# Kernel optimization log

Measured on AMD Instinct MI355X. Metric: run time of the kernel, lower is better.

The kernel has to match this reference:

```python
import jax, jax.numpy as jnp
import numpy as np

CH = 1024
NH = 16
HD = CH // NH


def setup_inputs() -> dict:
    key = jax.random.key(0)
    k1, k2, k3 = jax.random.split(key, 3)
    x = jax.random.normal(k1, (8, 1024, CH), dtype=jnp.float32)
    # torch.nn.Linear weights are [out, in]; store as [in, out] for x @ W
    s = 1.0 / np.sqrt(CH)
    W_qkv = jax.random.uniform(k2, (CH, 3 * CH), dtype=jnp.float32, minval=-s, maxval=s)
    W_out = jax.random.uniform(k3, (CH, CH), dtype=jnp.float32, minval=-s, maxval=s)
    return {"x": x, "W_qkv": W_qkv, "W_out": W_out}


def reference(x, W_qkv, W_out):
    B, N, C = x.shape
    qkv = x @ W_qkv                                   # [B, N, 3C]
    q, k, v = jnp.split(qkv, 3, axis=-1)
    # [B, N, C] -> [B, H, N, D]
    def heads(t):
        return t.reshape(B, N, NH, HD).transpose(0, 2, 1, 3)
    q, k, v = heads(q), heads(k), heads(v)
    scale = 1.0 / np.sqrt(HD).astype(np.float32)
    scores = jnp.einsum('bhqd,bhkd->bhqk', q, k) * scale
    attn = jax.nn.softmax(scores, axis=-1)
    out = jnp.einsum('bhqk,bhkd->bhqd', attn, v)      # [B, H, N, D]
    out = out.transpose(0, 2, 1, 3).reshape(B, N, C)
    return out @ W_out
```

## Files before the change

kernel.cpp:

```cpp
#include <hip/hip_runtime.h>
#include <math.h>

#define NH 16
#define HD 64

typedef unsigned short u16;
typedef unsigned int   u32;
using bf16x8 = __attribute__((ext_vector_type(8))) short;
using f32x4  = __attribute__((ext_vector_type(4))) float;
using u16x8  = __attribute__((ext_vector_type(8))) unsigned short;
using u16x4  = __attribute__((ext_vector_type(4))) unsigned short;
using u32x2  = __attribute__((ext_vector_type(2))) unsigned int;

__device__ __forceinline__ u16 f2bf(float x) {
    u32 u = __float_as_uint(x);
    u32 r = (u + 0x7FFFu + ((u >> 16) & 1u)) >> 16;
    return (u16)r;
}
__device__ __forceinline__ float bf2f(u16 h) { return __uint_as_float(((u32)h) << 16); }

#define GLDS16(src, dst) __builtin_amdgcn_global_load_lds( \
    (const __attribute__((address_space(1))) void*)(src),  \
    (__attribute__((address_space(3))) void*)(dst), 16, 0, 0)

#define LDS_OFF(p) ((u32)(uintptr_t)(__attribute__((address_space(3))) void*)(p))
#define DSREAD(d, a) asm volatile("ds_read_b128 %0, %1" : "=v"(d) : "v"(a))

#define MEMFENCE asm volatile("" ::: "memory")
#define BARMID { MEMFENCE; __builtin_amdgcn_s_barrier(); \
                 asm volatile("s_waitcnt lgkmcnt(0)" ::: "memory"); \
                 __builtin_amdgcn_sched_barrier(0); }
#define BAREND { MEMFENCE; __builtin_amdgcn_s_barrier(); MEMFENCE; }
#define VMW(n) asm volatile("s_waitcnt vmcnt(" #n ")" ::: "memory")

__global__ __launch_bounds__(256) void convert_x(const float* __restrict__ x,
                                                 u16* __restrict__ xt) {
    int t = blockIdx.x * 256 + threadIdx.x;
    int m = t >> 7;
    int k = (t & 127) * 8;
    const float4* src = (const float4*)(x + (size_t)m * 1024 + k);
    float4 v0 = src[0], v1 = src[1];
    float vs[8] = {v0.x, v0.y, v0.z, v0.w, v1.x, v1.y, v1.z, v1.w};
    u16x8 hv;
    #pragma unroll
    for (int j = 0; j < 8; j++) hv[j] = f2bf(vs[j]);
    *(u16x8*)(xt + (size_t)m * 1024 + k) = hv;
}

__global__ __launch_bounds__(256) void conv_w(const float* __restrict__ W,
                                              u16* __restrict__ wqk,
                                              u16* __restrict__ wv) {
    __shared__ float Ts[32][33];
    const int N = 3072;
    int k0 = blockIdx.y * 32, n0 = blockIdx.x * 32;
    int t = threadIdx.x;
    int r = t >> 3, c4 = (t & 7) * 4;
    float4 v = *(const float4*)(W + (size_t)(k0 + r) * N + n0 + c4);
    Ts[r][c4] = v.x; Ts[r][c4 + 1] = v.y; Ts[r][c4 + 2] = v.z; Ts[r][c4 + 3] = v.w;
    __syncthreads();
    int nl = t >> 3, kl = (t & 7) * 4;
    u16x4 hv;
    #pragma unroll
    for (int j = 0; j < 4; j++) hv[j] = f2bf(Ts[kl + j][nl]);
    int col = n0 + nl;
    if (col < 2048) {
        *(u16x4*)&wqk[(size_t)col * 1024 + k0 + kl] = hv;
    } else {
        *(u16x4*)&wv[(size_t)(col - 2048) * 1024 + k0 + kl] = hv;
    }
}

__global__ __launch_bounds__(256) void conv_wout(const float* __restrict__ W,
                                                 u16* __restrict__ Wt) {
    __shared__ float Ts[32][33];
    const int N = 1024;
    int k0 = blockIdx.y * 32, n0 = blockIdx.x * 32;
    int t = threadIdx.x;
    int r = t >> 3, c4 = (t & 7) * 4;
    float4 v = *(const float4*)(W + (size_t)(k0 + r) * N + n0 + c4);
    Ts[r][c4] = v.x; Ts[r][c4 + 1] = v.y; Ts[r][c4 + 2] = v.z; Ts[r][c4 + 3] = v.w;
    __syncthreads();
    int nl = t >> 3, kl = (t & 7) * 4;
    u16x4 hv;
    #pragma unroll
    for (int j = 0; j < 4; j++) hv[j] = f2bf(Ts[kl + j][nl]);
    *(u16x4*)&Wt[(size_t)(n0 + nl) * 1024 + k0 + kl] = hv;
}

__global__ __launch_bounds__(512, 2)
void gemm_qk_8ph(const u16* __restrict__ A, const u16* __restrict__ Bt,
                 u16* __restrict__ Qh, u16* __restrict__ Kh,
                 int Kp, int nbx) {
    __shared__ char LDS[131072];
    char* ldsA = LDS;
    char* ldsB = LDS + 65536;
    const u32 ldsAoff = LDS_OFF(ldsA);
    const u32 ldsBoff = ldsAoff + 65536;

    const int tid = threadIdx.x, lane = tid & 63, w = tid >> 6;
    const int wr = w >> 2, wc = w & 3;
    const int l15 = lane & 15;
    const int khb = (lane >> 4) << 4;
    const int lswz = (l15 & 7) << 4;
    const int Kp2 = Kp * 2;

    const int cpx = (int)gridDim.x >> 3;
    const int wg  = ((int)blockIdx.x & 7) * cpx + ((int)blockIdx.x >> 3);
    const int m0 = (wg / nbx) * 256, n0 = (wg % nbx) * 256;

    const int tp = tid >> 3;
    const int sw = ((tid & 7) * 16) ^ ((tp & 7) << 4);
    const int nA = ((tp >> 5) << 6) + (tp & 31);

    const char* Agb = (const char*)A  + (size_t)m0 * Kp2;
    const char* Bgb = (const char*)Bt + (size_t)n0 * Kp2;

#define STAGE_A(t, h, buf) { \
    const char* s_ = Agb + (t) * 128 + ((h) * 64 + tp) * Kp2 + sw; \
    char* d_ = ldsA + (buf) * 32768 + (h) * 16384 + (w << 10); \
    GLDS16(s_, d_); GLDS16(s_ + (size_t)128 * Kp2, d_ + 8192); }
#define STAGE_B(t, h, buf) { \
    const char* s_ = Bgb + (t) * 128 + (nA + (h) * 32) * Kp2 + sw; \
    char* d_ = ldsB + (buf) * 32768 + (h) * 16384 + (w << 10); \
    GLDS16(s_, d_); GLDS16(s_ + (size_t)128 * Kp2, d_ + 8192); }

    bf16x8 Af[4][2], Bf[2][2];

#define LOADA(buf, mh) { \
    _Pragma("unroll") \
    for (int mi = 0; mi < 4; ++mi) { \
        u32 rb_ = ldsAoff + (buf) * 32768 + (mh) * 16384 \
                + (u32)((wr * 64 + mi * 16 + l15) * 128); \
        DSREAD(Af[mi][0], rb_ + (u32)((khb) ^ lswz)); \
        DSREAD(Af[mi][1], rb_ + (u32)((64 + khb) ^ lswz)); \
    } }
#define LOADB(buf, nh) { \
    _Pragma("unroll") \
    for (int ni = 0; ni < 2; ++ni) { \
        u32 rb_ = ldsBoff + (buf) * 32768 + (nh) * 16384 \
                + (u32)((wc * 32 + ni * 16 + l15) * 128); \
        DSREAD(Bf[ni][0], rb_ + (u32)((khb) ^ lswz)); \
        DSREAD(Bf[ni][1], rb_ + (u32)((64 + khb) ^ lswz)); \
    } }
#define MM(mh, nh) { \
    __builtin_amdgcn_s_setprio(1); \
    _Pragma("unroll") \
    for (int kk = 0; kk < 2; ++kk) \
        _Pragma("unroll") \
        for (int mi = 0; mi < 4; ++mi) \
            _Pragma("unroll") \
            for (int ni = 0; ni < 2; ++ni) \
                acc[(mh) * 4 + mi][(nh) * 2 + ni] = \
                    __builtin_amdgcn_mfma_f32_16x16x32_bf16( \
                        Af[mi][kk], Bf[ni][kk], acc[(mh) * 4 + mi][(nh) * 2 + ni], 0, 0, 0); \
    __builtin_amdgcn_s_setprio(0); }

    f32x4 acc[8][4];
    #pragma unroll
    for (int i = 0; i < 8; i++)
        #pragma unroll
        for (int j = 0; j < 4; j++)
            acc[i][j] = f32x4{0.f, 0.f, 0.f, 0.f};

    const int NT = Kp >> 6;
    const int NITER = NT / 2 - 1;

    STAGE_B(0, 0, 0); STAGE_A(0, 1, 0); STAGE_B(0, 1, 0); STAGE_A(0, 0, 0);
    STAGE_B(1, 0, 1); STAGE_A(1, 1, 1); STAGE_B(1, 1, 1);
    VMW(6);
    MEMFENCE; __builtin_amdgcn_s_barrier(); MEMFENCE;

    for (int it = 0; it < NITER; ++it) {
        const int t = 2 * it;
        LOADA(0, 0); LOADB(0, 0); STAGE_A(t + 1, 0, 1);
        BARMID; MM(0, 0); BAREND;
        LOADA(0, 1); STAGE_B(t + 2, 0, 0);
        BARMID; MM(1, 0); BAREND;
        LOADB(0, 1); STAGE_A(t + 2, 1, 0);
        BARMID; MM(1, 1); BAREND;
        LOADA(0, 0); STAGE_B(t + 2, 1, 0); VMW(6);
        BARMID; MM(0, 1); BAREND;
        LOADA(1, 0); LOADB(1, 0); STAGE_A(t + 2, 0, 0);
        BARMID; MM(0, 0); BAREND;
        LOADA(1, 1); STAGE_B(t + 3, 0, 1);
        BARMID; MM(1, 0); BAREND;
        LOADB(1, 1); STAGE_A(t + 3, 1, 1);
        BARMID; MM(1, 1); BAREND;
        LOADA(1, 0); STAGE_B(t + 3, 1, 1); VMW(6);
        BARMID; MM(0, 1); BAREND;
    }

    LOADA(0, 0); LOADB(0, 0); STAGE_A(NT - 1, 0, 1);
    BARMID; MM(0, 0); BAREND;
    LOADA(0, 1);
    BARMID; MM(1, 0); BAREND;
    LOADB(0, 1);
    BARMID; MM(1, 1); BAREND;
    LOADA(0, 0); VMW(0);
    BARMID; MM(0, 1); BAREND;
    LOADA(1, 0); LOADB(1, 0);
    BARMID; MM(0, 0); BAREND;
    LOADA(1, 1);
    BARMID; MM(1, 0); BAREND;
    LOADB(1, 1);
    BARMID; MM(1, 1); BAREND;
    LOADA(1, 0);
    BARMID; MM(0, 1); BAREND;

    const int sel = n0 >> 10;
    u16* dst = (sel == 0) ? Qh : Kh;
    const float sc = (sel == 0) ? 0.125f : 1.0f;
    #pragma unroll
    for (int mh = 0; mh < 2; ++mh)
        #pragma unroll
        for (int mi = 0; mi < 4; ++mi)
            #pragma unroll
            for (int nh = 0; nh < 2; ++nh)
                #pragma unroll
                for (int ni = 0; ni < 2; ++ni) {
                    f32x4 a = acc[mh * 4 + mi][nh * 2 + ni];
                    int col = n0 + wc * 64 + nh * 32 + ni * 16 + l15;
                    int within = col & 1023;
                    int hh = within >> 6, d = within & 63;
                    int rowb = m0 + wr * 128 + mh * 64 + mi * 16 + (lane >> 4) * 4;
                    int bb = rowb >> 10, n = rowb & 1023;
                    size_t hn = (size_t)(bb * NH + hh) * 1024 + n;
                    #pragma unroll
                    for (int reg = 0; reg < 4; reg++)
                        dst[(hn + reg) * 64 + d] = f2bf(a[reg] * sc);
                }
#undef STAGE_A
#undef STAGE_B
#undef LOADA
#undef LOADB
#undef MM
}

template<int MODE>
__global__ __launch_bounds__(256, 2)
void gemm_bf16(const u16* __restrict__ A, int lda,
               const u16* __restrict__ Bt, int ldb, int Kloop,
               float* __restrict__ C, u16* __restrict__ Vtr, int N, int nbx) {
    __shared__ u16 As[128 * 64];
    __shared__ u16 Bs[128 * 64];
    const char* AsC = (const char*)As;
    const char* BsC = (const char*)Bs;

    const int t = threadIdx.x;
    const int lane = t & 63, w = t >> 6;

    const int cpx = (int)gridDim.x >> 3;
    const int wg  = (blockIdx.x & 7) * cpx + (blockIdx.x >> 3);
    const int m0 = (wg / nbx) * 128, n0 = (wg % nbx) * 128;

    const int l15 = lane & 15;
    const int g16 = (lane >> 4) << 4;
    const int swz = (l15 & 7) << 4;

    const char* srcA[4];
    const char* srcB[4];
    char* dstA[4];
    char* dstB[4];
    #pragma unroll
    for (int i = 0; i < 4; i++) {
        int s = (w * 4 + i) * 64 + lane;
        int row  = (s * 16) >> 7;
        int colb = (s * 16) & 127;
        int scol = colb ^ ((row & 7) << 4);
        srcA[i] = (const char*)A  + ((size_t)(m0 + row) * lda) * 2 + scol;
        srcB[i] = (const char*)Bt + ((size_t)(n0 + row) * ldb) * 2 + scol;
        dstA[i] = (char*)As + (w * 4 + i) * 1024;
        dstB[i] = (char*)Bs + (w * 4 + i) * 1024;
    }

    const int wm = (w >> 1) * 64, wn = (w & 1) * 64;
    int rA[4], rB[4];
    #pragma unroll
    for (int i = 0; i < 4; i++) {
        rA[i] = (wm + i * 16 + l15) * 128;
        rB[i] = (wn + i * 16 + l15) * 128;
    }

    f32x4 acc[4][4];
    #pragma unroll
    for (int i = 0; i < 4; i++)
        #pragma unroll
        for (int j = 0; j < 4; j++)
            acc[i][j] = f32x4{0.f, 0.f, 0.f, 0.f};

    for (int k0 = 0; k0 < Kloop; k0 += 64) {
        __syncthreads();
        #pragma unroll
        for (int i = 0; i < 4; i++) {
            GLDS16(srcA[i], dstA[i]);
            GLDS16(srcB[i], dstB[i]);
            srcA[i] += 128;
            srcB[i] += 128;
        }
        __syncthreads();
        #pragma unroll
        for (int kb = 0; kb < 2; kb++) {
            const int csw = ((kb << 6) | g16) ^ swz;
            bf16x8 af[4], bfr[4];
            #pragma unroll
            for (int mi = 0; mi < 4; mi++) af[mi]  = *(const bf16x8*)(AsC + rA[mi] + csw);
            #pragma unroll
            for (int ni = 0; ni < 4; ni++) bfr[ni] = *(const bf16x8*)(BsC + rB[ni] + csw);
            #pragma unroll
            for (int mi = 0; mi < 4; mi++)
                #pragma unroll
                for (int ni = 0; ni < 4; ni++)
                    acc[mi][ni] = __builtin_amdgcn_mfma_f32_16x16x32_bf16(
                        af[mi], bfr[ni], acc[mi][ni], 0, 0, 0);
        }
    }

    if (MODE == 0) {
        #pragma unroll
        for (int mi = 0; mi < 4; mi++) {
            int rowb = m0 + wm + mi * 16 + (lane >> 4) * 4;
            #pragma unroll
            for (int ni = 0; ni < 4; ni++) {
                int col = n0 + wn + ni * 16 + l15;
                #pragma unroll
                for (int reg = 0; reg < 4; reg++)
                    C[(size_t)(rowb + reg) * N + col] = acc[mi][ni][reg];
            }
        }
    } else {
        #pragma unroll
        for (int ni = 0; ni < 4; ni++) {
            int col = n0 + wn + ni * 16 + l15;
            int hh = col >> 6, d = col & 63;
            #pragma unroll
            for (int mi = 0; mi < 4; mi++) {
                int rowb = m0 + wm + mi * 16 + (lane >> 4) * 4;
                int bb = rowb >> 10, n = rowb & 1023;
                u16x4 vv;
                #pragma unroll
                for (int reg = 0; reg < 4; reg++)
                    vv[reg] = f2bf(acc[mi][ni][reg]);
                *(u16x4*)&Vtr[((size_t)(bb * NH + hh) * 64 + d) * 1024 + n] = vv;
            }
        }
    }
}

__global__ __launch_bounds__(256, 4)
void attn_mfma(const u16* __restrict__ Qh, const u16* __restrict__ Kh,
               const u16* __restrict__ Vt, u16* __restrict__ AO) {
    __shared__ u16 Ks[64 * 64];
    __shared__ u16 Vs[64 * 64];
    __shared__ u16 Ps[4][16 * 72];

    const int t = threadIdx.x, lane = t & 63, w = t >> 6;

    const int orig = blockIdx.x;
    const int xcd = orig & 7, slot = orig >> 3;
    const int head_lin = xcd * 16 + (slot >> 4);
    const int qt = slot & 15;
    const int b = head_lin >> 4, h = head_lin & 15;
    const size_t head = (size_t)head_lin;

    const char* Qg = (const char*)(Qh + head * 1024 * 64) + qt * 64 * 128;
    const char* Kg = (const char*)(Kh + head * 1024 * 64);
    const char* Vg = (const char*)(Vt + head * 64 * 1024);
    char* KsC = (char*)Ks;
    char* VsC = (char*)Vs;
    char* PsC = (char*)(&Ps[w][0]);

    const int l15 = lane & 15;
    const int g16 = (lane >> 4) << 4;
    const int g8  = (lane >> 4) << 3;
    const int swz = (l15 & 7) << 4;

    #pragma unroll
    for (int i = 0; i < 2; i++) {
        int c = (w * 2 + i) * 64 + lane;
        int row = c >> 3, colb = (c & 7) * 16;
        int off = row * 128 + (colb ^ ((row & 7) << 4));
        GLDS16(Kg + off, KsC + (w * 2 + i) * 1024);
        GLDS16(Vg + row * 2048 + (colb ^ ((row & 7) << 4)), VsC + (w * 2 + i) * 1024);
    }

    const int qrow = w * 16 + l15;
    bf16x8 qf[2];
    #pragma unroll
    for (int kk = 0; kk < 2; kk++)
        qf[kk] = *(const bf16x8*)(Qg + qrow * 128 + kk * 64 + g16);

    int ksrcoff[2], kdst[2], vsrcoff[2], vdst[2];
    #pragma unroll
    for (int i = 0; i < 2; i++) {
        int c = i * 256 + t;
        int row = c >> 3, colb = (c & 7) * 16;
        ksrcoff[i] = c * 16;
        kdst[i]    = row * 128 + (colb ^ ((row & 7) << 4));
        vsrcoff[i] = row * 2048 + colb;
        vdst[i]    = row * 128 + (colb ^ ((row & 7) << 4));
    }

    float lp = 0.f;
    f32x4 acc_o[4];
    #pragma unroll
    for (int i = 0; i < 4; i++) acc_o[i] = f32x4{0.f, 0.f, 0.f, 0.f};

    __syncthreads();

    for (int kt = 0; kt < 16; kt++) {
        u16x8 kst[2], vst[2];
        if (kt < 15) {
            const char* ks = Kg + (kt + 1) * 8192;
            const char* vs = Vg + (kt + 1) * 128;
            #pragma unroll
            for (int i = 0; i < 2; i++) {
                kst[i] = *(const u16x8*)(ks + ksrcoff[i]);
                vst[i] = *(const u16x8*)(vs + vsrcoff[i]);
            }
        }

        f32x4 sacc[4];
        #pragma unroll
        for (int c = 0; c < 4; c++) sacc[c] = f32x4{0.f, 0.f, 0.f, 0.f};
        __builtin_amdgcn_s_setprio(1);
        #pragma unroll
        for (int kk = 0; kk < 2; kk++) {
            int csw = ((kk * 64) | g16) ^ swz;
            #pragma unroll
            for (int c = 0; c < 4; c++) {
                bf16x8 bk = *(const bf16x8*)(KsC + (c * 16 + l15) * 128 + csw);
                sacc[c] = __builtin_amdgcn_mfma_f32_16x16x32_bf16(bk, qf[kk], sacc[c], 0, 0, 0);
            }
        }
        __builtin_amdgcn_s_setprio(0);

        {
            char* pb = PsC + l15 * 144 + g8;
            #pragma unroll
            for (int c = 0; c < 4; c++) {
                float p0 = __expf(sacc[c][0]);
                float p1 = __expf(sacc[c][1]);
                float p2 = __expf(sacc[c][2]);
                float p3 = __expf(sacc[c][3]);
                lp += (p0 + p1) + (p2 + p3);
                u32 w0, w1;
                asm("v_cvt_pk_bf16_f32 %0, %1, %2" : "=v"(w0) : "v"(p0), "v"(p1));
                asm("v_cvt_pk_bf16_f32 %0, %1, %2" : "=v"(w1) : "v"(p2), "v"(p3));
                u16x4 pk = __builtin_bit_cast(u16x4, u32x2{w0, w1});
                *(u16x4*)(pb + c * 32) = pk;
            }
        }
        MEMFENCE;
        asm volatile("s_waitcnt lgkmcnt(0)" ::: "memory");
        __builtin_amdgcn_sched_barrier(0);

        __builtin_amdgcn_s_setprio(1);
        #pragma unroll
        for (int kb = 0; kb < 2; kb++) {
            bf16x8 ap = *(const bf16x8*)(PsC + l15 * 144 + kb * 64 + g16);
            #pragma unroll
            for (int c2 = 0; c2 < 4; c2++) {
                int vrow = c2 * 16 + l15;
                int voff = vrow * 128 + (((kb << 6) | g16) ^ ((vrow & 7) << 4));
                bf16x8 bv = *(const bf16x8*)(VsC + voff);
                acc_o[c2] = __builtin_amdgcn_mfma_f32_16x16x32_bf16(ap, bv, acc_o[c2], 0, 0, 0);
            }
        }
        __builtin_amdgcn_s_setprio(0);

        __syncthreads();
        if (kt < 15) {
            #pragma unroll
            for (int i = 0; i < 2; i++) {
                *(u16x8*)(KsC + kdst[i]) = kst[i];
                *(u16x8*)(VsC + vdst[i]) = vst[i];
            }
            __syncthreads();
        }
    }

    lp += __shfl_xor(lp, 16, 64);
    lp += __shfl_xor(lp, 32, 64);
    float linv[4];
    #pragma unroll
    for (int reg = 0; reg < 4; reg++)
        linv[reg] = 1.0f / __shfl(lp, ((lane >> 4) << 2) + reg, 64);

    #pragma unroll
    for (int c2 = 0; c2 < 4; c2++) {
        int col = h * 64 + c2 * 16 + l15;
        #pragma unroll
        for (int reg = 0; reg < 4; reg++) {
            int row = b * 1024 + qt * 64 + w * 16 + (lane >> 4) * 4 + reg;
            float v = acc_o[c2][reg] * linv[reg];
            AO[(size_t)row * 1024 + col] = f2bf(v);
        }
    }
}

extern "C" void kernel_launch(void* const* d_in, const int* in_sizes, int n_in,
                              void* d_out, int out_size, void* d_ws, size_t ws_size,
                              hipStream_t stream) {
    const float* x    = (const float*)d_in[0];
    const float* Wqkv = (const float*)d_in[1];
    const float* Wout = (const float*)d_in[2];
    float* out = (float*)d_out;

    u16* xt    = (u16*)d_ws;
    u16* wqk   = xt + 8192ull * 1024;
    u16* wv    = wqk + 2048ull * 1024;
    u16* woutt = wv + 1024ull * 1024;
    u16* Qh    = woutt + 1024ull * 1024;
    u16* Kh    = Qh + 128ull * 1024 * 64;
    u16* Vtr   = Kh + 128ull * 1024 * 64;
    u16* AO    = xt;

    convert_x<<<4096, 256, 0, stream>>>(x, xt);
    conv_w<<<dim3(96, 32), 256, 0, stream>>>(Wqkv, wqk, wv);
    conv_wout<<<dim3(32, 32), 256, 0, stream>>>(Wout, woutt);

    gemm_qk_8ph<<<256, 512, 0, stream>>>(xt, wqk, Qh, Kh, 1024, 8);

    gemm_bf16<2><<<512, 256, 0, stream>>>(
        xt, 1024, wv, 1024, 1024, nullptr, Vtr, 1024, 8);

    attn_mfma<<<2048, 256, 0, stream>>>(Qh, Kh, Vtr, AO);

    gemm_bf16<0><<<512, 256, 0, stream>>>(
        AO, 1024, woutt, 1024, 1024, out, nullptr, 1024, 8);
}
```

Before: 154.4 us.

## Double-buffer attention K/V tiles with direct global-to-LDS loads and exp2 softmax

The attention kernel now keeps two LDS buffers for K and V. The next tile is fetched straight into the spare buffer with global_load_lds, replacing the old register staging plus an extra write-and-sync phase. This removes one barrier per iteration and the register round-trip, at the cost of twice the K/V shared memory, and the occupancy hint drops from 4 to 3 blocks. Separately, log2(e) is folded into the Q scaling in the projection kernel so the softmax can use exp2f instead of __expf.

```diff
diff --git a/kernel.cpp b/kernel.cpp
--- a/kernel.cpp
+++ b/kernel.cpp
@@ -209,7 +209,7 @@
 
     const int sel = n0 >> 10;
     u16* dst = (sel == 0) ? Qh : Kh;
-    const float sc = (sel == 0) ? 0.125f : 1.0f;
+    const float sc = (sel == 0) ? 0.125f * 1.4426950408889634f : 1.0f;
     #pragma unroll
     for (int mh = 0; mh < 2; ++mh)
         #pragma unroll
@@ -346,11 +346,11 @@
     }
 }
 
-__global__ __launch_bounds__(256, 4)
+__global__ __launch_bounds__(256, 3)
 void attn_mfma(const u16* __restrict__ Qh, const u16* __restrict__ Kh,
                const u16* __restrict__ Vt, u16* __restrict__ AO) {
-    __shared__ u16 Ks[64 * 64];
-    __shared__ u16 Vs[64 * 64];
+    __shared__ u16 Ks[2][64 * 64];
+    __shared__ u16 Vs[2][64 * 64];
     __shared__ u16 Ps[4][16 * 72];
 
     const int t = threadIdx.x, lane = t & 63, w = t >> 6;
@@ -372,16 +372,24 @@
     const int l15 = lane & 15;
     const int g16 = (lane >> 4) << 4;
     const int g8  = (lane >> 4) << 3;
-    const int swz = (l15 & 7) << 4;
-
+
+    int koff[2], vgoff[2], ldst[2];
     #pragma unroll
     for (int i = 0; i < 2; i++) {
         int c = (w * 2 + i) * 64 + lane;
         int row = c >> 3, colb = (c & 7) * 16;
-        int off = row * 128 + (colb ^ ((row & 7) << 4));
-        GLDS16(Kg + off, KsC + (w * 2 + i) * 1024);
-        GLDS16(Vg + row * 2048 + (colb ^ ((row & 7) << 4)), VsC + (w * 2 + i) * 1024);
-    }
+        int soff = colb ^ ((row & 7) << 4);
+        koff[i]  = row * 128 + soff;
+        vgoff[i] = row * 2048 + soff;
+        ldst[i]  = (w * 2 + i) * 1024;
+    }
+
+#define STAGE_KV(kt, buf) { \
+    _Pragma("unroll") \
+    for (int i = 0; i < 2; i++) { \
+        GLDS16(Kg + (kt) * 8192 + koff[i], KsC + (buf) * 8192 + ldst[i]); \
+        GLDS16(Vg + (kt) * 128  + vgoff[i], VsC + (buf) * 8192 + ldst[i]); \
+    } }
 
     const int qrow = w * 16 + l15;
     bf16x8 qf[2];
@@ -389,35 +397,17 @@
     for (int kk = 0; kk < 2; kk++)
         qf[kk] = *(const bf16x8*)(Qg + qrow * 128 + kk * 64 + g16);
 
-    int ksrcoff[2], kdst[2], vsrcoff[2], vdst[2];
-    #pragma unroll
-    for (int i = 0; i < 2; i++) {
-        int c = i * 256 + t;
-        int row = c >> 3, colb = (c & 7) * 16;
-        ksrcoff[i] = c * 16;
-        kdst[i]    = row * 128 + (colb ^ ((row & 7) << 4));
-        vsrcoff[i] = row * 2048 + colb;
-        vdst[i]    = row * 128 + (colb ^ ((row & 7) << 4));
-    }
-
     float lp = 0.f;
     f32x4 acc_o[4];
     #pragma unroll
     for (int i = 0; i < 4; i++) acc_o[i] = f32x4{0.f, 0.f, 0.f, 0.f};
 
+    STAGE_KV(0, 0);
     __syncthreads();
 
     for (int kt = 0; kt < 16; kt++) {
-        u16x8 kst[2], vst[2];
-        if (kt < 15) {
-            const char* ks = Kg + (kt + 1) * 8192;
-            const char* vs = Vg + (kt + 1) * 128;
-            #pragma unroll
-            for (int i = 0; i < 2; i++) {
-                kst[i] = *(const u16x8*)(ks + ksrcoff[i]);
-                vst[i] = *(const u16x8*)(vs + vsrcoff[i]);
-            }
-        }
+        const int cur = kt & 1;
+        if (kt < 15) STAGE_KV(kt + 1, cur ^ 1);
 
         f32x4 sacc[4];
         #pragma unroll
@@ -425,10 +415,10 @@
         __builtin_amdgcn_s_setprio(1);
         #pragma unroll
         for (int kk = 0; kk < 2; kk++) {
-            int csw = ((kk * 64) | g16) ^ swz;
+            int csw = ((kk * 64) | g16) ^ ((l15 & 7) << 4);
             #pragma unroll
             for (int c = 0; c < 4; c++) {
-                bf16x8 bk = *(const bf16x8*)(KsC + (c * 16 + l15) * 128 + csw);
+                bf16x8 bk = *(const bf16x8*)(KsC + cur * 8192 + (c * 16 + l15) * 128 + csw);
                 sacc[c] = __builtin_amdgcn_mfma_f32_16x16x32_bf16(bk, qf[kk], sacc[c], 0, 0, 0);
             }
         }
@@ -438,10 +428,10 @@
             char* pb = PsC + l15 * 144 + g8;
             #pragma unroll
             for (int c = 0; c < 4; c++) {
-                float p0 = __expf(sacc[c][0]);
-                float p1 = __expf(sacc[c][1]);
-                float p2 = __expf(sacc[c][2]);
-                float p3 = __expf(sacc[c][3]);
+                float p0 = exp2f(sacc[c][0]);
+                float p1 = exp2f(sacc[c][1]);
+                float p2 = exp2f(sacc[c][2]);
+                float p3 = exp2f(sacc[c][3]);
                 lp += (p0 + p1) + (p2 + p3);
                 u32 w0, w1;
                 asm("v_cvt_pk_bf16_f32 %0, %1, %2" : "=v"(w0) : "v"(p0), "v"(p1));
@@ -462,22 +452,15 @@
             for (int c2 = 0; c2 < 4; c2++) {
                 int vrow = c2 * 16 + l15;
                 int voff = vrow * 128 + (((kb << 6) | g16) ^ ((vrow & 7) << 4));
-                bf16x8 bv = *(const bf16x8*)(VsC + voff);
+                bf16x8 bv = *(const bf16x8*)(VsC + cur * 8192 + voff);
                 acc_o[c2] = __builtin_amdgcn_mfma_f32_16x16x32_bf16(ap, bv, acc_o[c2], 0, 0, 0);
             }
         }
         __builtin_amdgcn_s_setprio(0);
 
-        __syncthreads();
-        if (kt < 15) {
-            #pragma unroll
-            for (int i = 0; i < 2; i++) {
-                *(u16x8*)(KsC + kdst[i]) = kst[i];
-                *(u16x8*)(VsC + vdst[i]) = vst[i];
-            }
-            __syncthreads();
-        }
-    }
+        if (kt < 15) __syncthreads();
+    }
+#undef STAGE_KV
 
     lp += __shfl_xor(lp, 16, 64);
     lp += __shfl_xor(lp, 32, 64);
```

New measurement: 163.0 us. +5.6%, slower.
